# Kernel optimization log

Measured on AMD Instinct MI355X. Metric: run time of the kernel, lower is better.

The kernel has to match this reference:

```python
import jax, jax.numpy as jnp
import numpy as np

K = 24          # SiFinder.KERNEL_SIZE
SIGMA = 1e-6    # SiFinder.CORR_SIGMA


def setup_inputs() -> dict:
    key = jax.random.key(0)
    k1, k2, k3 = jax.random.split(key, 3)
    H = W = 480
    x_dec = jax.random.normal(k1, (1, 3, H, W), dtype=jnp.float32)
    y_dec = jax.random.normal(k2, (1, 3, H, W), dtype=jnp.float32)
    y = jax.random.normal(k3, (1, 3, H, W), dtype=jnp.float32)
    return {"x_dec": x_dec, "y_dec": y_dec, "y": y}


def _get_x_patches(x_dec):
    # non-overlapping KxK patches, raster order (rows of patches, then cols)
    _, C, H, W = x_dec.shape
    p = x_dec[0].reshape(C, H // K, K, W // K, K)
    return p.transpose(1, 3, 0, 2, 4).reshape(-1, C, K, K)  # (P, C, K, K)


def _conv(img, w):
    # valid cross-correlation, matches F.conv2d
    return jax.lax.conv_general_dilated(
        img, w, window_strides=(1, 1), padding='VALID',
        dimension_numbers=('NCHW', 'OIHW', 'NCHW'))


def _pearson_corr(x_patches, y):
    C = x_patches.shape[1]
    ps = C * K * K  # patch_size
    mean_x = jnp.mean(x_patches, axis=(1, 2, 3))[None, :, None, None]   # (1,P,1,1)
    sum_x2 = jnp.sum(x_patches ** 2, axis=(1, 2, 3))[None, :, None, None]
    ones = jnp.ones((1, C, K, K), y.dtype)
    sum_y = _conv(y, ones)            # (1,1,H',W'); torch builds P identical channels
    xy = _conv(y, x_patches)          # (1,P,H',W')
    numer = xy / ps - mean_x * sum_y / ps
    den_x = sum_x2 / ps - mean_x ** 2
    den_y = _conv(y ** 2, ones) / ps - sum_y ** 2 / ps ** 2
    return (2 * numer + SIGMA) / (jnp.abs(den_x) + jnp.abs(den_y) + SIGMA)


def _forward(x_dec, y_dec, y):
    x_patches = _get_x_patches(x_dec)
    corr = _pearson_corr(x_patches, y_dec)          # (1, P, H', W')
    _, P, Hc, Wc = corr.shape
    idx = jnp.argmax(corr[0].reshape(P, Hc * Wc), axis=-1)
    rows, cols = idx // Wc, idx % Wc
    # roi_align(boxes=[-0.5+c, -0.5+r, ...], out=KxK, sampling_ratio=-1) samples
    # exactly at integer pixel centers -> reduces to an exact patch gather from y.
    C = y.shape[1]
    def take(r, c):
        return jax.lax.dynamic_slice(y[0], (0, r, c), (C, K, K))
    patches = jax.vmap(take)(rows, cols)            # (P, C, K, K)
    # nn.Fold with stride==kernel: stitch non-overlapping patches back to image
    H, W = x_dec.shape[2], x_dec.shape[3]
    img = patches.reshape(H // K, W // K, C, K, K).transpose(2, 0, 3, 1, 4)
    return img.reshape(1, C, H, W)


def reference(x_dec, y_dec, y):
    return _forward(x_dec, y_dec, y)
```

## Files before the change

### kernel.cpp

```cpp
#include <hip/hip_runtime.h>
#include <stdint.h>

#define HW    480
#define KS    24
#define CH    3
#define HO    457
#define NPOS  (HO*HO)
#define NP    400
#define PS    (CH*KS*KS)
#define SIG   1e-6f
#define NSQ   54
#define NMT   14
#define NIY   115
#define NGRP  (NIY*8*4)
#define MAXF  16384
#define RGRID 4096
#define DELTA 4e-3f
#define QS    28.0f
#define IS2   (1.0f/(QS*QS))
#define PB    2608

typedef __attribute__((ext_vector_type(4)))  int  int4v;
typedef __attribute__((ext_vector_type(16))) int  int16v;
typedef unsigned int uint;
typedef unsigned char uchar;
typedef unsigned long long ull;

static __device__ __forceinline__ char q8(float v) {
    float s = rintf(v * QS);
    s = fminf(127.f, fmaxf(-127.f, s));
    return (char)(int)s;
}
static __device__ __forceinline__ uint mono(float f) {
    uint u = __float_as_uint(f);
    return (u & 0x80000000u) ? ~u : (u | 0x80000000u);
}
static __device__ __forceinline__ float unmono(uint u) {
    uint b = (u & 0x80000000u) ? (u & 0x7fffffffu) : ~u;
    return __uint_as_float(b);
}

__global__ void fat1_k(const float* __restrict__ x, const float* __restrict__ yd,
                       float* __restrict__ Wp, char* __restrict__ yq,
                       float* __restrict__ cs, float* __restrict__ cs2) {
    int b = blockIdx.x;
    if (b < 2700) {
        int t = b * 256 + threadIdx.x;
        int p = t / PS, e = t - p * PS;
        int c = e / (KS * KS);
        int r = (e / KS) % KS;
        int w = e % KS;
        int pr = p / 20, pc = p - pr * 20;
        Wp[t] = x[c * HW * HW + (pr * KS + r) * HW + (pc * KS + w)];
    } else if (b < 5400) {
        int t = (b - 2700) * 256 + threadIdx.x;
        yq[t] = q8(yd[t]);
    } else {
        int t = (b - 5400) * 256 + threadIdx.x;
        if (t >= HO * HW) return;
        int i = t / HW, w = t - i * HW;
        float s = 0.f, s2 = 0.f;
        for (int c = 0; c < CH; c++) {
            const float* base = yd + c * HW * HW + i * HW + w;
            for (int dh = 0; dh < KS; dh++) {
                float v = base[dh * HW];
                s += v; s2 += v * v;
            }
        }
        cs[t] = s; cs2[t] = s2;
    }
}

__global__ void fat2_k(const float* __restrict__ Wp,
                       const float* __restrict__ cs, const float* __restrict__ cs2,
                       float* __restrict__ meanX, float* __restrict__ denXa,
                       char* __restrict__ Aq,
                       float* __restrict__ sumY, float* __restrict__ denYa,
                       uint* __restrict__ cnt, ull* __restrict__ best) {
    __shared__ float shs[4], shs2[4];
    int b = blockIdx.x;
    if (b < 400) {
        int p = b;
        if (threadIdx.x == 1) best[p] = 0ull;
        if (b == 0 && threadIdx.x == 2) *cnt = 0u;
        float s = 0.f, s2 = 0.f;
        for (int e = threadIdx.x; e < PS; e += 256) {
            float v = Wp[p * PS + e];
            s += v; s2 += v * v;
        }
        for (int o = 32; o > 0; o >>= 1) { s += __shfl_down(s, o); s2 += __shfl_down(s2, o); }
        int lane = threadIdx.x & 63, wv = threadIdx.x >> 6;
        if (lane == 0) { shs[wv] = s; shs2[wv] = s2; }
        __syncthreads();
        if (threadIdx.x == 0) {
            float S = shs[0] + shs[1] + shs[2] + shs[3];
            float S2 = shs2[0] + shs2[1] + shs2[2] + shs2[3];
            float m = S / (float)PS;
            meanX[p] = m;
            denXa[p] = fabsf(S2 / (float)PS - m * m);
        }
    } else if (b < 3424) {
        int id = (b - 400) * 256 + threadIdx.x;
        int e    = id & 15;
        int lane = (id >> 4) & 63;
        int f    = id >> 10;
        int s    = f % NSQ;
        int mtg  = f / NSQ;
        int kk = s * 32 + (lane >> 5) * 16 + e;
        int p  = mtg * 32 + (lane & 31);
        float v = (p < NP) ? Wp[p * PS + kk] : 0.f;
        Aq[id] = q8(v);
    } else {
        int t = (b - 3424) * 256 + threadIdx.x;
        if (t >= NPOS) return;
        int i = t / HO, j = t - i * HO;
        const float* r  = cs  + i * HW + j;
        const float* r2 = cs2 + i * HW + j;
        float s = 0.f, s2 = 0.f;
        for (int d = 0; d < KS; d++) { s += r[d]; s2 += r2[d]; }
        sumY[t] = s;
        float ips = 1.0f / (float)PS;
        denYa[t] = fabsf(s2 * ips - (s * ips) * (s * ips));
    }
}

__launch_bounds__(256, 3)
__global__ void corr1_k(const char* __restrict__ yq, const char* __restrict__ Aq,
                        const float* __restrict__ meanX, const float* __restrict__ denXa,
                        const float* __restrict__ sumY, const float* __restrict__ denYa,
                        uint* __restrict__ table) {
    __shared__ __align__(16) uchar S[8 * PB];

    const int tid  = threadIdx.x;
    const int lane = tid & 63;
    const int g    = tid >> 6;
    const int n    = lane & 31;
    const int kha  = lane >> 5;
    const int jx   = blockIdx.x;
    const int iy   = blockIdx.y;
    const int mtp  = blockIdx.z;
    const int j0   = 64 * jx;
    const int i0   = 4 * iy;
    const int i    = i0 + g;

    const int olo0 = kha ? 16  : 0,   ohi0 = kha ? 96  : 8;
    const int olo1 = kha ? 192 : 104, ohi1 = kha ? 200 : 112;
    const int olo2 = kha ? 296 : 208, ohi2 = kha ? 304 : 288;

    const uchar* Bt0g = S + ((2 * n) & 7) * PB + ((2 * n) & ~7) + g * 96;
    const uchar* Bt1g = Bt0g + PB;

    const char* A0 = Aq + ((size_t)(mtp * 2 + 0) * NSQ << 10) + lane * 16;
    const char* A1 = Aq + ((size_t)(mtp * 2 + 1) * NSQ << 10) + lane * 16;

    int16v acc[2][2];
#pragma unroll
    for (int mt = 0; mt < 2; mt++)
#pragma unroll
        for (int t = 0; t < 2; t++) acc[mt][t] = (int16v)0;

    for (int c = 0; c < CH; c++) {
        __syncthreads();
        for (int it = tid; it < 27 * 6; it += 256) {
            int row = it / 6;
            int gb  = (it - row * 6) * 16;
            int yr  = i0 + row;
            int gj  = j0 + gb;
            uint d[6];
            if (yr < HW && gj + 24 <= HW) {
                const uchar* src = (const uchar*)yq + ((size_t)(c * HW + yr)) * HW + gj;
                uint4 a = *(const uint4*)src;
                uint2 bb = *(const uint2*)(src + 16);
                d[0] = a.x; d[1] = a.y; d[2] = a.z; d[3] = a.w; d[4] = bb.x; d[5] = bb.y;
            } else {
                uchar tmp[24];
#pragma unroll
                for (int e = 0; e < 24; e++) {
                    int col = gj + e;
                    tmp[e] = (yr < HW && col < HW)
                           ? ((const uchar*)yq)[((size_t)(c * HW + yr)) * HW + col] : (uchar)0;
                }
                const uint* tp = (const uint*)tmp;
#pragma unroll
                for (int e = 0; e < 6; e++) d[e] = tp[e];
            }
            int base = row * 96 + gb;
#pragma unroll
            for (int pi = 0; pi < 8; pi++) {
                const int a = pi >> 2;
                const int r = pi & 3;
                uint4 w;
                if (r == 0)
                    w = make_uint4(d[a], d[a + 1], d[a + 2], d[a + 3]);
                else
                    w = make_uint4((d[a]     >> (8 * r)) | (d[a + 1] << (32 - 8 * r)),
                                   (d[a + 1] >> (8 * r)) | (d[a + 2] << (32 - 8 * r)),
                                   (d[a + 2] >> (8 * r)) | (d[a + 3] << (32 - 8 * r)),
                                   (d[a + 3] >> (8 * r)) | (d[a + 4] << (32 - 8 * r)));
                *(uint4*)&S[pi * PB + base] = w;
            }
        }
        __syncthreads();

        const char* A0c = A0 + ((size_t)(c * 18) << 10);
        const char* A1c = A1 + ((size_t)(c * 18) << 10);
        for (int q = 0; q < 6; q++) {
            const char* A0q = A0c + ((size_t)(3 * q) << 10);
            const char* A1q = A1c + ((size_t)(3 * q) << 10);
            int4v a0v[3], a1v[3];
#pragma unroll
            for (int u = 0; u < 3; u++) {
                a0v[u] = *(const int4v*)(A0q + (u << 10));
                a1v[u] = *(const int4v*)(A1q + (u << 10));
            }
            const uchar* Bq0 = Bt0g + 384 * q;
            const uchar* Bq1 = Bt1g + 384 * q;
#pragma unroll
            for (int u = 0; u < 3; u++) {
                const int olo = (u == 0) ? olo0 : (u == 1) ? olo1 : olo2;
                const int ohi = (u == 0) ? ohi0 : (u == 1) ? ohi1 : ohi2;
#pragma unroll
                for (int t = 0; t < 2; t++) {
                    const uchar* Bq = t ? Bq1 : Bq0;
                    uint2 lo = *(const uint2*)(Bq + olo);
                    uint2 hi = *(const uint2*)(Bq + ohi);
                    int4v bv;
                    bv.x = (int)lo.x; bv.y = (int)lo.y; bv.z = (int)hi.x; bv.w = (int)hi.y;
                    acc[0][t] = __builtin_amdgcn_mfma_i32_32x32x32_i8(a0v[u], bv, acc[0][t], 0, 0, 0);
                    acc[1][t] = __builtin_amdgcn_mfma_i32_32x32x32_i8(a1v[u], bv, acc[1][t], 0, 0, 0);
                }
            }
        }
    }

    const int grp = (iy * 8 + jx) * 4 + g;
    const float c2 = 2.0f / (float)PS;
    const bool iok = i < HO;
    float sYv[2], rDv[2];
#pragma unroll
    for (int t = 0; t < 2; t++) {
        int j = j0 + 2 * n + t;
        bool ok = iok && (j < HO);
        sYv[t] = ok ? sumY[i * HO + j] : 0.f;
        rDv[t] = ok ? denYa[i * HO + j] : 0.f;
    }
    const bool jv0 = iok && (j0 + 2 * n + 0 < HO);
    const bool jv1 = iok && (j0 + 2 * n + 1 < HO);
#pragma unroll
    for (int mt = 0; mt < 2; mt++) {
        const int pbase = (mtp * 2 + mt) * 32;
#pragma unroll
        for (int r = 0; r < 16; r++) {
            int p = pbase + (r & 3) + 8 * (r >> 2) + 4 * kha;
            bool pok = p < NP;
            float mX = pok ? meanX[p] : 0.f;
            float dX = pok ? denXa[p] : 0.f;
            float bu = -3.0e38f;
#pragma unroll
            for (int t = 0; t < 2; t++) {
                bool ok = t ? jv1 : jv0;
                if (ok) {
                    float xy = (float)acc[mt][t][r] * IS2;
                    float numer = fmaf(-mX, sYv[t], xy) * c2 + SIG;
                    float rp = __builtin_amdgcn_rcpf(dX + rDv[t] + SIG);
                    bu = fmaxf(bu, numer * rp);
                }
            }
#pragma unroll
            for (int o = 1; o < 32; o <<= 1)
                bu = fmaxf(bu, __shfl_xor(bu, o));
            if (n == 0 && pok) table[p * NGRP + grp] = mono(bu);
        }
    }
}

__global__ void flag_k(const uint* __restrict__ table,
                       uint* __restrict__ flags, uint* __restrict__ cnt) {
    __shared__ uint sm[4];
    __shared__ float sthr;
    int p = blockIdx.x;
    uint m = 0;
    for (int g = threadIdx.x; g < NGRP; g += 256) {
        uint v = table[p * NGRP + g];
        m = v > m ? v : m;
    }
    for (int o = 32; o > 0; o >>= 1) { uint ot = __shfl_down(m, o); m = ot > m ? ot : m; }
    int lane = threadIdx.x & 63, wv = threadIdx.x >> 6;
    if (lane == 0) sm[wv] = m;
    __syncthreads();
    if (threadIdx.x == 0) {
        uint mm = max(max(sm[0], sm[1]), max(sm[2], sm[3]));
        sthr = unmono(mm) - DELTA;
    }
    __syncthreads();
    float thr = sthr;
    for (int g = threadIdx.x; g < NGRP; g += 256) {
        if (unmono(table[p * NGRP + g]) >= thr) {
            uint idx = atomicAdd(cnt, 1u);
            if (idx < MAXF) flags[idx] = (uint)(p * NGRP + g);
        }
    }
}

__launch_bounds__(64)
__global__ void rescore_k(const float* __restrict__ Wp, const float* __restrict__ y_dec,
                          const float* __restrict__ meanX, const float* __restrict__ denXa,
                          const float* __restrict__ sumY, const float* __restrict__ denYa,
                          const uint* __restrict__ flags, const uint* __restrict__ cnt,
                          ull* __restrict__ best) {
    uint nflag = *cnt; if (nflag > MAXF) nflag = MAXF;
    for (uint fb = blockIdx.x; fb < nflag; fb += RGRID) {
        uint f = flags[fb];
        int p = f / NGRP, grp = f - p * NGRP;
        int g = grp & 3, bj = grp >> 2;
        int jx = bj & 7, iy = bj >> 3;
        int i = 4 * iy + g;
        int j = 64 * jx + threadIdx.x;
        ull pk = 0;
        if (i < HO && j < HO) {
            float dot = 0.f;
            const float* wr = Wp + p * PS;
            for (int c = 0; c < CH; c++)
                for (int kh = 0; kh < KS; kh++) {
                    const float* yr = y_dec + ((c * HW) + i + kh) * HW + j;
                    const float* wk = wr + (c * KS + kh) * KS;
#pragma unroll
                    for (int kw = 0; kw < KS; kw++) dot += wk[kw] * yr[kw];
                }
            float corr = (2.0f * (dot - meanX[p] * sumY[i * HO + j]) * (1.0f / (float)PS) + SIG)
                       / (denXa[p] + denYa[i * HO + j] + SIG);
            uint idx = (uint)(i * HO + j);
            pk = ((ull)mono(corr) << 32) | (uint)(~idx);
        }
        for (int o = 32; o > 0; o >>= 1) { ull ot = __shfl_down(pk, o); pk = ot > pk ? ot : pk; }
        if (threadIdx.x == 0) atomicMax(&best[p], pk);
    }
}

__global__ void gather_k(const float* __restrict__ y,
                         const ull* __restrict__ best,
                         float* __restrict__ out) {
    int p = blockIdx.x;
    uint idx = ~((uint)(best[p] & 0xFFFFFFFFull));
    int r = idx / HO, cc = idx - r * HO;
    int pr = p / 20, pc = p - pr * 20;
    for (int e = threadIdx.x; e < PS; e += 256) {
        int c = e / (KS * KS);
        int kh = (e / KS) % KS;
        int kw = e % KS;
        out[c * HW * HW + (pr * KS + kh) * HW + (pc * KS + kw)] =
            y[c * HW * HW + (r + kh) * HW + (cc + kw)];
    }
}

extern "C" void kernel_launch(void* const* d_in, const int* in_sizes, int n_in,
                              void* d_out, int out_size, void* d_ws, size_t ws_size,
                              hipStream_t stream) {
    const float* x_dec = (const float*)d_in[0];
    const float* y_dec = (const float*)d_in[1];
    const float* y     = (const float*)d_in[2];
    float* out = (float*)d_out;

    char* ws = (char*)d_ws;
    size_t off = 0;
    auto carve = [&](size_t bytes) -> void* {
        void* p = ws + off;
        off += (bytes + 255) & ~(size_t)255;
        return p;
    };
    float*  Wp    = (float*)carve((size_t)NP * PS * 4);
    char*   yq    = (char*)carve((size_t)CH * HW * HW);
    char*   Aq    = (char*)carve((size_t)NMT * NSQ * 1024);
    float*  cs    = (float*)carve((size_t)HO * HW * 4);
    float*  cs2   = (float*)carve((size_t)HO * HW * 4);
    float*  sumY  = (float*)carve((size_t)NPOS * 4);
    float*  denYa = (float*)carve((size_t)NPOS * 4);
    float*  meanX = (float*)carve((size_t)NP * 4);
    float*  denXa = (float*)carve((size_t)NP * 4);
    uint*   table = (uint*)carve((size_t)NP * NGRP * 4);
    uint*   flags = (uint*)carve((size_t)MAXF * 4);
    uint*   cnt   = (uint*)carve(256);
    ull*    best  = (ull*)carve((size_t)NP * 8);

    fat1_k<<<6257, 256, 0, stream>>>(x_dec, y_dec, Wp, yq, cs, cs2);
    fat2_k<<<4240, 256, 0, stream>>>(Wp, cs, cs2, meanX, denXa, Aq, sumY, denYa, cnt, best);

    dim3 grid(8, NIY, 7);
    corr1_k<<<grid, 256, 0, stream>>>(yq, Aq, meanX, denXa, sumY, denYa, table);

    flag_k<<<NP, 256, 0, stream>>>(table, flags, cnt);
    rescore_k<<<RGRID, 64, 0, stream>>>(Wp, y_dec, meanX, denXa, sumY, denYa, flags, cnt, best);

    gather_k<<<NP, 256, 0, stream>>>(y, best, out);
}
```

Measured before the change: 401.5 us.

## Widen corr1 M-tiling to four patch tiles per block for B reuse

Templates the int8 MFMA correlation body on the number of 32-patch M-tiles per block. Most blocks now handle four tiles and the last handles two, so the grid z dimension drops from 7 to 4 and each block's shared-memory staging of the quantized y image is shared across more patches. B fragments are now loaded once up front per q step and reused across all M-tiles. The cost is more accumulator and A registers per thread, with launch bounds lowered from 3 to 2 blocks per SM, which reduces occupancy.

```diff
diff --git a/kernel.cpp b/kernel.cpp
--- a/kernel.cpp
+++ b/kernel.cpp
@@ -124,13 +124,13 @@
     }
 }
 
-__launch_bounds__(256, 3)
-__global__ void corr1_k(const char* __restrict__ yq, const char* __restrict__ Aq,
-                        const float* __restrict__ meanX, const float* __restrict__ denXa,
-                        const float* __restrict__ sumY, const float* __restrict__ denYa,
-                        uint* __restrict__ table) {
-    __shared__ __align__(16) uchar S[8 * PB];
-
+template<int MT>
+static __device__ __forceinline__ void corr1_body(
+        const int mt0,
+        const char* __restrict__ yq, const char* __restrict__ Aq,
+        const float* __restrict__ meanX, const float* __restrict__ denXa,
+        const float* __restrict__ sumY, const float* __restrict__ denYa,
+        uint* __restrict__ table, uchar* __restrict__ S) {
     const int tid  = threadIdx.x;
     const int lane = tid & 63;
     const int g    = tid >> 6;
@@ -138,24 +138,21 @@
     const int kha  = lane >> 5;
     const int jx   = blockIdx.x;
     const int iy   = blockIdx.y;
-    const int mtp  = blockIdx.z;
     const int j0   = 64 * jx;
     const int i0   = 4 * iy;
     const int i    = i0 + g;
 
-    const int olo0 = kha ? 16  : 0,   ohi0 = kha ? 96  : 8;
-    const int olo1 = kha ? 192 : 104, ohi1 = kha ? 200 : 112;
-    const int olo2 = kha ? 296 : 208, ohi2 = kha ? 304 : 288;
+    const int olo[3] = { kha ? 16  : 0,   kha ? 192 : 104, kha ? 296 : 208 };
+    const int ohi[3] = { kha ? 96  : 8,   kha ? 200 : 112, kha ? 304 : 288 };
 
     const uchar* Bt0g = S + ((2 * n) & 7) * PB + ((2 * n) & ~7) + g * 96;
     const uchar* Bt1g = Bt0g + PB;
 
-    const char* A0 = Aq + ((size_t)(mtp * 2 + 0) * NSQ << 10) + lane * 16;
-    const char* A1 = Aq + ((size_t)(mtp * 2 + 1) * NSQ << 10) + lane * 16;
-
-    int16v acc[2][2];
-#pragma unroll
-    for (int mt = 0; mt < 2; mt++)
+    const char* Ab = Aq + ((size_t)mt0 * NSQ << 10) + lane * 16;
+
+    int16v acc[MT][2];
+#pragma unroll
+    for (int mt = 0; mt < MT; mt++)
 #pragma unroll
         for (int t = 0; t < 2; t++) acc[mt][t] = (int16v)0;
 
@@ -202,34 +199,37 @@
         }
         __syncthreads();
 
-        const char* A0c = A0 + ((size_t)(c * 18) << 10);
-        const char* A1c = A1 + ((size_t)(c * 18) << 10);
+        const char* Ac = Ab + ((size_t)(c * 18) << 10);
         for (int q = 0; q < 6; q++) {
-            const char* A0q = A0c + ((size_t)(3 * q) << 10);
-            const char* A1q = A1c + ((size_t)(3 * q) << 10);
-            int4v a0v[3], a1v[3];
-#pragma unroll
-            for (int u = 0; u < 3; u++) {
-                a0v[u] = *(const int4v*)(A0q + (u << 10));
-                a1v[u] = *(const int4v*)(A1q + (u << 10));
-            }
+            const char* Aqp = Ac + ((size_t)(3 * q) << 10);
+            int4v av[MT][3];
+#pragma unroll
+            for (int mt = 0; mt < MT; mt++)
+#pragma unroll
+                for (int u = 0; u < 3; u++)
+                    av[mt][u] = *(const int4v*)(Aqp + mt * (NSQ << 10) + (u << 10));
+
             const uchar* Bq0 = Bt0g + 384 * q;
             const uchar* Bq1 = Bt1g + 384 * q;
+            uint2 blo[3][2], bhi[3][2];
 #pragma unroll
             for (int u = 0; u < 3; u++) {
-                const int olo = (u == 0) ? olo0 : (u == 1) ? olo1 : olo2;
-                const int ohi = (u == 0) ? ohi0 : (u == 1) ? ohi1 : ohi2;
+                blo[u][0] = *(const uint2*)(Bq0 + olo[u]);
+                bhi[u][0] = *(const uint2*)(Bq0 + ohi[u]);
+                blo[u][1] = *(const uint2*)(Bq1 + olo[u]);
+                bhi[u][1] = *(const uint2*)(Bq1 + ohi[u]);
+            }
+#pragma unroll
+            for (int u = 0; u < 3; u++)
 #pragma unroll
                 for (int t = 0; t < 2; t++) {
-                    const uchar* Bq = t ? Bq1 : Bq0;
-                    uint2 lo = *(const uint2*)(Bq + olo);
-                    uint2 hi = *(const uint2*)(Bq + ohi);
                     int4v bv;
-                    bv.x = (int)lo.x; bv.y = (int)lo.y; bv.z = (int)hi.x; bv.w = (int)hi.y;
-                    acc[0][t] = __builtin_amdgcn_mfma_i32_32x32x32_i8(a0v[u], bv, acc[0][t], 0, 0, 0);
-                    acc[1][t] = __builtin_amdgcn_mfma_i32_32x32x32_i8(a1v[u], bv, acc[1][t], 0, 0, 0);
+                    bv.x = (int)blo[u][t].x; bv.y = (int)blo[u][t].y;
+                    bv.z = (int)bhi[u][t].x; bv.w = (int)bhi[u][t].y;
+#pragma unroll
+                    for (int mt = 0; mt < MT; mt++)
+                        acc[mt][t] = __builtin_amdgcn_mfma_i32_32x32x32_i8(av[mt][u], bv, acc[mt][t], 0, 0, 0);
                 }
-            }
         }
     }
 
@@ -247,8 +247,8 @@
     const bool jv0 = iok && (j0 + 2 * n + 0 < HO);
     const bool jv1 = iok && (j0 + 2 * n + 1 < HO);
 #pragma unroll
-    for (int mt = 0; mt < 2; mt++) {
-        const int pbase = (mtp * 2 + mt) * 32;
+    for (int mt = 0; mt < MT; mt++) {
+        const int pbase = (mt0 + mt) * 32;
 #pragma unroll
         for (int r = 0; r < 16; r++) {
             int p = pbase + (r & 3) + 8 * (r >> 2) + 4 * kha;
@@ -272,6 +272,18 @@
             if (n == 0 && pok) table[p * NGRP + grp] = mono(bu);
         }
     }
+}
+
+__launch_bounds__(256, 2)
+__global__ void corr1_k(const char* __restrict__ yq, const char* __restrict__ Aq,
+                        const float* __restrict__ meanX, const float* __restrict__ denXa,
+                        const float* __restrict__ sumY, const float* __restrict__ denYa,
+                        uint* __restrict__ table) {
+    __shared__ __align__(16) uchar S[8 * PB];
+    if (blockIdx.z == 3)
+        corr1_body<2>(12, yq, Aq, meanX, denXa, sumY, denYa, table, S);
+    else
+        corr1_body<4>(4 * blockIdx.z, yq, Aq, meanX, denXa, sumY, denYa, table, S);
 }
 
 __global__ void flag_k(const uint* __restrict__ table,
@@ -385,7 +397,7 @@
     fat1_k<<<6257, 256, 0, stream>>>(x_dec, y_dec, Wp, yq, cs, cs2);
     fat2_k<<<4240, 256, 0, stream>>>(Wp, cs, cs2, meanX, denXa, Aq, sumY, denYa, cnt, best);
 
-    dim3 grid(8, NIY, 7);
+    dim3 grid(8, NIY, 4);
     corr1_k<<<grid, 256, 0, stream>>>(yq, Aq, meanX, denXa, sumY, denYa, table);
 
     flag_k<<<NP, 256, 0, stream>>>(table, flags, cnt);
```

New measurement: 429.8 us. +7.1%, slower.
